# Kernel optimization log

Hardware: AMD Instinct MI355X
Metric: run time of the kernel (lower is better)

Reference implementation:

```python
import jax, jax.numpy as jnp
import numpy as np


def setup_inputs() -> dict:
    key = jax.random.key(0)
    k1, k2 = jax.random.split(key)
    token_inputs = jax.random.normal(k1, (4, 2048, 4096), dtype=jnp.float32)
    w_gate = jax.random.normal(k2, (4096, 64), dtype=jnp.float32)
    return {"token_inputs": token_inputs, "w_gate": w_gate, "expert_capacity": 40}


def reference(token_inputs, w_gate, expert_capacity):
    # Gating: [b, n, d] @ [d, e] -> [b, n, e]
    router_logits = jnp.einsum('bnd,de->bne', token_inputs, w_gate)

    # Router z-loss: mean of squared logsumexp over experts.
    z_loss = jnp.mean(jax.nn.logsumexp(router_logits, axis=-1) ** 2)

    router_probs = jax.nn.softmax(router_logits, axis=-1)
    num_experts = router_probs.shape[-1]

    # Top-1 (Switch) routing.
    expert_index = jnp.argmax(router_probs, axis=-1)          # [b, n]
    expert_gate = jnp.max(router_probs, axis=-1)              # [b, n]
    expert_mask = jax.nn.one_hot(expert_index, num_experts,
                                 dtype=router_probs.dtype)    # [b, n, e]

    # Load-balancing auxiliary loss.
    density = jnp.mean(expert_mask, axis=1)                   # [b, e] dispatch fraction
    density_proxy = jnp.mean(router_probs, axis=1)            # [b, e] mean prob
    aux_loss = jnp.mean(density * density_proxy) * (num_experts ** 2)

    # Capacity assignment via cumulative sum over tokens (0-based slot index).
    position_in_expert = (jnp.cumsum(expert_mask, axis=1) - 1.0) * expert_mask  # [b, n, e]
    within_capacity = (position_in_expert < expert_capacity).astype(router_probs.dtype) * expert_mask

    pos_idx = position_in_expert.astype(jnp.int32)            # [b, n, e]
    # Dispatch: one-hot over capacity slots, zeroed for dropped tokens. [b, n, e, c]
    dispatch_tensor = within_capacity[..., None] * jax.nn.one_hot(
        pos_idx, expert_capacity, dtype=router_probs.dtype)
    # Combine: dispatch scaled by the router gate probability.
    combine_tensor = dispatch_tensor * expert_gate[:, :, None, None]

    return dispatch_tensor, combine_tensor, aux_loss, z_loss
```

## Files before the change

kernel.cpp:

```cpp
#include <hip/hip_runtime.h>
#include <stdint.h>

#define B_    4
#define N_    2048
#define D_    4096
#define E_    64
#define TOKENS (B_ * N_)
#define KT    32
#define TM    128
#define KS    8
#define KCHUNK (D_ / KS)
#define NITER (KCHUNK / KT)

typedef float vfloat4 __attribute__((ext_vector_type(4)));

#define GL2LDS16(g, s) __builtin_amdgcn_global_load_lds(                     \
    (const __attribute__((address_space(1))) void*)(g),                      \
    (__attribute__((address_space(3))) void*)(s), 16, 0, 0)

__global__ __launch_bounds__(256) void k_gemm_z(const float* __restrict__ A,
                                                const float* __restrict__ W,
                                                float* __restrict__ P,
                                                float* __restrict__ out,
                                                float* __restrict__ probsum,
                                                float* __restrict__ losses) {
    __shared__ float As[2][TM][KT];
    __shared__ float Ws[2][KT][E_];

    const int tid   = threadIdx.x;
    const int l     = tid & 63;
    const int w     = tid >> 6;
    const int tok0  = blockIdx.x * TM;
    const int kc    = blockIdx.y;
    const int kbase = kc * KCHUNK;
    const int blin  = kc * gridDim.x + blockIdx.x;

    const int t0 = (tid >> 4) * 8;
    const int e0 = (tid & 15) * 4;
    const int sw = (tid >> 4) & 7;

    const float* pA[4];
    #pragma unroll
    for (int q = 0; q < 4; ++q) {
        const int i  = w * 4 + q;
        const int tk = i * 8 + (l >> 3);
        const int ks = (l & 7) ^ (i & 7);
        pA[q] = A + (size_t)(tok0 + tk) * D_ + kbase + ks * 4;
    }
    const float* pW[2];
    #pragma unroll
    for (int q = 0; q < 2; ++q) {
        const int j  = w * 2 + q;
        const int kk = j * 4 + (l >> 4);
        pW[q] = W + (size_t)(kbase + kk) * E_ + (l & 15) * 4;
    }

    vfloat4* zbase = reinterpret_cast<vfloat4*>(out) + (size_t)blin * 20480 + tid;
    const vfloat4 z4 = {0.f, 0.f, 0.f, 0.f};

    if (blin == 0) {
        probsum[tid] = 0.f;
        if (tid < 2) losses[tid] = 0.f;
    }

    #pragma unroll
    for (int q = 0; q < 4; ++q) {
        GL2LDS16(pA[q], &As[0][(w * 4 + q) * 8][0]);
        pA[q] += KT;
    }
    #pragma unroll
    for (int q = 0; q < 2; ++q) {
        GL2LDS16(pW[q], &Ws[0][(w * 2 + q) * 4][0]);
        pW[q] += KT * E_;
    }
    __syncthreads();

    float acc[8][4];
    #pragma unroll
    for (int i = 0; i < 8; ++i)
        #pragma unroll
        for (int j = 0; j < 4; ++j) acc[i][j] = 0.f;

    #pragma unroll 1
    for (int kt = 0; kt < NITER; ++kt) {
        const int cur = kt & 1;
        const int nxt = cur ^ 1;

        if (kt + 1 < NITER) {
            #pragma unroll
            for (int q = 0; q < 4; ++q) {
                GL2LDS16(pA[q], &As[nxt][(w * 4 + q) * 8][0]);
                pA[q] += KT;
            }
            #pragma unroll
            for (int q = 0; q < 2; ++q) {
                GL2LDS16(pW[q], &Ws[nxt][(w * 2 + q) * 4][0]);
                pW[q] += KT * E_;
            }
        }

        #pragma unroll
        for (int j = 0; j < 5; ++j)
            __builtin_nontemporal_store(z4, zbase + (size_t)(kt * 5 + j) * 256);

        #pragma unroll
        for (int kk4 = 0; kk4 < 8; ++kk4) {
            float4 av[8];
            const int so = ((kk4 ^ sw) << 2);
            #pragma unroll
            for (int i = 0; i < 8; ++i)
                av[i] = *reinterpret_cast<const float4*>(&As[cur][t0 + i][so]);
            #pragma unroll
            for (int k = 0; k < 4; ++k) {
                const float4 w0 = *reinterpret_cast<const float4*>(&Ws[cur][kk4 * 4 + k][e0]);
                #pragma unroll
                for (int i = 0; i < 8; ++i) {
                    const float a = (k == 0) ? av[i].x : (k == 1) ? av[i].y
                                  : (k == 2) ? av[i].z : av[i].w;
                    acc[i][0] += a * w0.x; acc[i][1] += a * w0.y;
                    acc[i][2] += a * w0.z; acc[i][3] += a * w0.w;
                }
            }
        }
        __syncthreads();
    }

    float* base = P + ((size_t)kc * TOKENS + tok0) * E_;
    #pragma unroll
    for (int i = 0; i < 8; ++i)
        *reinterpret_cast<float4*>(&base[(size_t)(t0 + i) * E_ + e0]) =
            make_float4(acc[i][0], acc[i][1], acc[i][2], acc[i][3]);
}

__global__ __launch_bounds__(256) void k_softmax(const float* __restrict__ P,
                                                 int* __restrict__ idx,
                                                 float* __restrict__ gate,
                                                 float* __restrict__ probsum,
                                                 float* __restrict__ out_z) {
    const int tid  = threadIdx.x;
    const int wid  = tid >> 6;
    const int lane = tid & 63;
    const int tok0 = blockIdx.x * 32 + wid * 8;

    float ps = 0.f;
    float zz = 0.f;

    #pragma unroll
    for (int t = 0; t < 8; ++t) {
        const int tok = tok0 + t;

        float l = 0.f;
        #pragma unroll
        for (int kc = 0; kc < KS; ++kc)
            l += P[((size_t)kc * TOKENS + tok) * E_ + lane];

        float m = l; int mi = lane;
        #pragma unroll
        for (int off = 32; off > 0; off >>= 1) {
            const float om = __shfl_down(m, off);
            const int   oi = __shfl_down(mi, off);
            if (om > m || (om == m && oi < mi)) { m = om; mi = oi; }
        }
        m  = __shfl(m, 0);
        mi = __shfl(mi, 0);

        const float p = __expf(l - m);
        float s = p;
        #pragma unroll
        for (int off = 32; off > 0; off >>= 1) s += __shfl_down(s, off);
        s = __shfl(s, 0);

        ps += p / s;
        if (lane == 0) {
            const float lse = m + logf(s);
            zz += lse * lse;
            idx[tok]  = mi;
            gate[tok] = 1.0f / s;
        }
    }

    __shared__ float pacc[4][E_];
    __shared__ float zv[4];
    pacc[wid][lane] = ps;
    if (lane == 0) zv[wid] = zz;
    __syncthreads();

    if (tid < E_) {
        const float v = pacc[0][tid] + pacc[1][tid] + pacc[2][tid] + pacc[3][tid];
        const int b = (blockIdx.x * 32) / N_;
        atomicAdd(&probsum[b * E_ + tid], v);
    }
    if (tid == 0)
        atomicAdd(out_z, (zv[0] + zv[1] + zv[2] + zv[3]) * (1.0f / (float)TOKENS));
}

__global__ __launch_bounds__(64) void k_posloss(const int* __restrict__ idx,
                                                const float* __restrict__ gate,
                                                const float* __restrict__ probsum,
                                                float* __restrict__ out,
                                                float* __restrict__ out_aux,
                                                int C, size_t half) {
    const int b = blockIdx.x >> 6;
    const int e = blockIdx.x & 63;
    const int lane = threadIdx.x;
    const int*   ib = idx  + b * N_;
    const float* gb = gate + b * N_;
    float* ob = out + (size_t)b * N_ * E_ * C;

    int running = 0;
    for (int step = 0; step < N_ / 64; ++step) {
        const int t = step * 64 + lane;
        const bool match = (ib[t] == e);
        const unsigned long long mask = __ballot(match);
        if (match) {
            const int p = running + __popcll(mask & ((1ull << lane) - 1ull));
            if (p < C) {
                const size_t off = (size_t)t * E_ * C + (size_t)e * C + p;
                ob[off] = 1.0f;
                ob[half + off] = gb[t];
            }
        }
        running += __popcll(mask);
    }
    if (lane == 0)
        atomicAdd(out_aux,
                  (float)running * probsum[b * E_ + e] * (1.0f / 262144.0f));
}

extern "C" void kernel_launch(void* const* d_in, const int* in_sizes, int n_in,
                              void* d_out, int out_size, void* d_ws, size_t ws_size,
                              hipStream_t stream) {
    const float* A = (const float*)d_in[0];
    const float* W = (const float*)d_in[1];
    float* out = (float*)d_out;

    const size_t half = ((size_t)out_size - 2) / 2;
    const int C = (int)(half / ((size_t)TOKENS * E_));

    float* P = (float*)d_ws;
    size_t off = (size_t)KS * TOKENS * E_;
    int*   idx     = (int*)(P + off);   off += TOKENS;
    float* gate    = P + off;           off += TOKENS;
    float* probsum = P + off;           off += B_ * E_;

    float* out_aux = out + 2 * half;
    float* out_z   = out + 2 * half + 1;

    k_gemm_z<<<dim3(TOKENS / TM, KS), 256, 0, stream>>>(A, W, P, out, probsum,
                                                        out_aux);
    k_softmax<<<TOKENS / 32, 256, 0, stream>>>(P, idx, gate, probsum, out_z);
    k_posloss<<<B_ * E_, 64, 0, stream>>>(idx, gate, probsum, out, out_aux, C, half);
}
```

Before: 318.8 us.

## Use single-wave GEMM blocks with 8x8 register tiles and barrier-free pipelining

The gating GEMM now runs one 64-thread wavefront per block over a 64-token tile, and each thread computes an 8x8 output tile instead of 8x4. With a single wave per block, the __syncthreads barriers give way to explicit vmcnt waits, and the double-buffered loads are issued partway through compute so they overlap with the FMAs. Zero-fill stores for the output are interleaved the same way. The cost is twice as many blocks, fewer waves per block, higher register pressure, and less W reuse across tokens per LDS load.

```diff
diff --git a/kernel.cpp b/kernel.cpp
--- a/kernel.cpp
+++ b/kernel.cpp
@@ -7,7 +7,7 @@
 #define E_    64
 #define TOKENS (B_ * N_)
 #define KT    32
-#define TM    128
+#define TM    64
 #define KS    8
 #define KCHUNK (D_ / KS)
 #define NITER (KCHUNK / KT)
@@ -18,118 +18,110 @@
     (const __attribute__((address_space(1))) void*)(g),                      \
     (__attribute__((address_space(3))) void*)(s), 16, 0, 0)
 
-__global__ __launch_bounds__(256) void k_gemm_z(const float* __restrict__ A,
-                                                const float* __restrict__ W,
-                                                float* __restrict__ P,
-                                                float* __restrict__ out,
-                                                float* __restrict__ probsum,
-                                                float* __restrict__ losses) {
+__global__ __launch_bounds__(64) void k_gemm_z(const float* __restrict__ A,
+                                               const float* __restrict__ W,
+                                               float* __restrict__ P,
+                                               float* __restrict__ out,
+                                               float* __restrict__ probsum,
+                                               float* __restrict__ losses) {
     __shared__ float As[2][TM][KT];
     __shared__ float Ws[2][KT][E_];
 
-    const int tid   = threadIdx.x;
-    const int l     = tid & 63;
-    const int w     = tid >> 6;
+    const int l     = threadIdx.x;
     const int tok0  = blockIdx.x * TM;
     const int kc    = blockIdx.y;
     const int kbase = kc * KCHUNK;
     const int blin  = kc * gridDim.x + blockIdx.x;
 
-    const int t0 = (tid >> 4) * 8;
-    const int e0 = (tid & 15) * 4;
-    const int sw = (tid >> 4) & 7;
-
-    const float* pA[4];
-    #pragma unroll
-    for (int q = 0; q < 4; ++q) {
-        const int i  = w * 4 + q;
-        const int tk = i * 8 + (l >> 3);
-        const int ks = (l & 7) ^ (i & 7);
-        pA[q] = A + (size_t)(tok0 + tk) * D_ + kbase + ks * 4;
-    }
-    const float* pW[2];
-    #pragma unroll
-    for (int q = 0; q < 2; ++q) {
-        const int j  = w * 2 + q;
-        const int kk = j * 4 + (l >> 4);
-        pW[q] = W + (size_t)(kbase + kk) * E_ + (l & 15) * 4;
-    }
-
-    vfloat4* zbase = reinterpret_cast<vfloat4*>(out) + (size_t)blin * 20480 + tid;
+    const int t0 = (l >> 3) * 8;
+    const int e0 = (l & 7) * 8;
+    const int sw = l >> 3;
+
+    const float* pA[8];
+    #pragma unroll
+    for (int i = 0; i < 8; ++i)
+        pA[i] = A + (size_t)(tok0 + i * 8 + (l >> 3)) * D_ + kbase
+                  + ((l & 7) ^ i) * 4;
+    const float* pW[8];
+    #pragma unroll
+    for (int j = 0; j < 8; ++j)
+        pW[j] = W + (size_t)(kbase + j * 4 + (l >> 4)) * E_ + (l & 15) * 4;
+
+    vfloat4* zbase = reinterpret_cast<vfloat4*>(out) + (size_t)blin * 10240 + l;
     const vfloat4 z4 = {0.f, 0.f, 0.f, 0.f};
 
     if (blin == 0) {
-        probsum[tid] = 0.f;
-        if (tid < 2) losses[tid] = 0.f;
-    }
-
-    #pragma unroll
-    for (int q = 0; q < 4; ++q) {
-        GL2LDS16(pA[q], &As[0][(w * 4 + q) * 8][0]);
-        pA[q] += KT;
-    }
-    #pragma unroll
-    for (int q = 0; q < 2; ++q) {
-        GL2LDS16(pW[q], &Ws[0][(w * 2 + q) * 4][0]);
-        pW[q] += KT * E_;
-    }
-    __syncthreads();
-
-    float acc[8][4];
+        #pragma unroll
+        for (int q = 0; q < 4; ++q) probsum[l + q * 64] = 0.f;
+        if (l < 2) losses[l] = 0.f;
+    }
+
+    float acc[8][8];
     #pragma unroll
     for (int i = 0; i < 8; ++i)
         #pragma unroll
-        for (int j = 0; j < 4; ++j) acc[i][j] = 0.f;
-
-    #pragma unroll 1
-    for (int kt = 0; kt < NITER; ++kt) {
-        const int cur = kt & 1;
-        const int nxt = cur ^ 1;
-
-        if (kt + 1 < NITER) {
-            #pragma unroll
-            for (int q = 0; q < 4; ++q) {
-                GL2LDS16(pA[q], &As[nxt][(w * 4 + q) * 8][0]);
-                pA[q] += KT;
-            }
-            #pragma unroll
-            for (int q = 0; q < 2; ++q) {
-                GL2LDS16(pW[q], &Ws[nxt][(w * 2 + q) * 4][0]);
-                pW[q] += KT * E_;
-            }
-        }
-
-        #pragma unroll
-        for (int j = 0; j < 5; ++j)
-            __builtin_nontemporal_store(z4, zbase + (size_t)(kt * 5 + j) * 256);
-
-        #pragma unroll
-        for (int kk4 = 0; kk4 < 8; ++kk4) {
+        for (int j = 0; j < 8; ++j) acc[i][j] = 0.f;
+
+    auto STAGE = [&](int b) {
+        #pragma unroll
+        for (int q = 0; q < 8; ++q) { GL2LDS16(pA[q], &As[b][q * 8][0]); pA[q] += KT; }
+        #pragma unroll
+        for (int q = 0; q < 8; ++q) { GL2LDS16(pW[q], &Ws[b][q * 4][0]); pW[q] += KT * E_; }
+    };
+    auto ZST = [&](int t) {
+        #pragma unroll
+        for (int j = 0; j < 10; ++j)
+            __builtin_nontemporal_store(z4, zbase + (size_t)(t * 10 + j) * 64);
+    };
+    auto COMPUTE = [&](int b, int lo, int hi) {
+        #pragma unroll
+        for (int kk4 = lo; kk4 < hi; ++kk4) {
             float4 av[8];
             const int so = ((kk4 ^ sw) << 2);
             #pragma unroll
             for (int i = 0; i < 8; ++i)
-                av[i] = *reinterpret_cast<const float4*>(&As[cur][t0 + i][so]);
+                av[i] = *reinterpret_cast<const float4*>(&As[b][t0 + i][so]);
             #pragma unroll
             for (int k = 0; k < 4; ++k) {
-                const float4 w0 = *reinterpret_cast<const float4*>(&Ws[cur][kk4 * 4 + k][e0]);
+                const float4 w0 = *reinterpret_cast<const float4*>(&Ws[b][kk4 * 4 + k][e0]);
+                const float4 w1 = *reinterpret_cast<const float4*>(&Ws[b][kk4 * 4 + k][e0 + 4]);
                 #pragma unroll
                 for (int i = 0; i < 8; ++i) {
                     const float a = (k == 0) ? av[i].x : (k == 1) ? av[i].y
                                   : (k == 2) ? av[i].z : av[i].w;
                     acc[i][0] += a * w0.x; acc[i][1] += a * w0.y;
                     acc[i][2] += a * w0.z; acc[i][3] += a * w0.w;
+                    acc[i][4] += a * w1.x; acc[i][5] += a * w1.y;
+                    acc[i][6] += a * w1.z; acc[i][7] += a * w1.w;
                 }
             }
         }
-        __syncthreads();
+    };
+
+    STAGE(0);
+
+    #pragma unroll 1
+    for (int kt = 0; kt < NITER; kt += 2) {
+        asm volatile("s_waitcnt vmcnt(0)" ::: "memory");
+        COMPUTE(0, 0, 4);
+        ZST(kt);
+        if (kt + 1 < NITER) STAGE(1);
+        COMPUTE(0, 4, 8);
+        asm volatile("s_waitcnt vmcnt(0)" ::: "memory");
+        COMPUTE(1, 0, 4);
+        ZST(kt + 1);
+        if (kt + 2 < NITER) STAGE(0);
+        COMPUTE(1, 4, 8);
     }
 
     float* base = P + ((size_t)kc * TOKENS + tok0) * E_;
     #pragma unroll
-    for (int i = 0; i < 8; ++i)
+    for (int i = 0; i < 8; ++i) {
         *reinterpret_cast<float4*>(&base[(size_t)(t0 + i) * E_ + e0]) =
             make_float4(acc[i][0], acc[i][1], acc[i][2], acc[i][3]);
+        *reinterpret_cast<float4*>(&base[(size_t)(t0 + i) * E_ + e0 + 4]) =
+            make_float4(acc[i][4], acc[i][5], acc[i][6], acc[i][7]);
+    }
 }
 
 __global__ __launch_bounds__(256) void k_softmax(const float* __restrict__ P,
@@ -246,8 +238,8 @@
     float* out_aux = out + 2 * half;
     float* out_z   = out + 2 * half + 1;
 
-    k_gemm_z<<<dim3(TOKENS / TM, KS), 256, 0, stream>>>(A, W, P, out, probsum,
-                                                        out_aux);
+    k_gemm_z<<<dim3(TOKENS / TM, KS), 64, 0, stream>>>(A, W, P, out, probsum,
+                                                       out_aux);
     k_softmax<<<TOKENS / 32, 256, 0, stream>>>(P, idx, gate, probsum, out_z);
     k_posloss<<<B_ * E_, 64, 0, stream>>>(idx, gate, probsum, out, out_aux, C, half);
 }
```

New measurement: 677.7 us. +112.6%, slower.
